# Kernel tuning notes

Measured on AMD Instinct MI355X. Metric: run time of the kernel, lower is better.

Reference implementation:

```python
import jax, jax.numpy as jnp
import numpy as np


def setup_inputs() -> dict:
    key = jax.random.key(0)
    ks = jax.random.split(key, 5)
    B, S, D, L = 16, 256, 768, 32
    return {
        "head": jax.random.normal(ks[0], (B, S, D), dtype=jnp.float32),
        "dep": jax.random.normal(ks[1], (B, S, D), dtype=jnp.float32),
        "label_U_diag": jax.random.normal(ks[2], (L, D), dtype=jnp.float32) * 0.02,
        "label_W": jax.random.normal(ks[3], (L, 2 * D), dtype=jnp.float32) * 0.02,
        "label_b": jax.random.normal(ks[4], (L,), dtype=jnp.float32) * 0.02,
    }


def reference(head, dep, label_U_diag, label_W, label_b):
    # head, dep: [b, s, d]; label_U_diag: [l, d]; label_W: [l, 2d]; label_b: [l]
    d = head.shape[-1]
    # Bilinear term with diagonal U: t1[b,l,i,o] = sum_d head[b,i,d]*U[l,d]*dep[b,o,d]
    t1 = jnp.einsum('bid,ld,bod->blio', head, label_U_diag, dep)
    # Linear term: W @ concat(head_i, dep_o) = W_h @ head_i + W_d @ dep_o
    W_h, W_d = label_W[:, :d], label_W[:, d:]
    t2_h = jnp.einsum('ld,bid->bli', W_h, head)  # [b, l, s]
    t2_d = jnp.einsum('ld,bod->blo', W_d, dep)   # [b, l, s]
    return t1 + t2_h[:, :, :, None] + t2_d[:, :, None, :] + label_b[None, :, None, None]
```

## Files before the change

kernel.cpp:

```cpp
#include <hip/hip_runtime.h>
#include <hip/hip_bf16.h>
#include <stdint.h>


#define B_ 16
#define S_ 256
#define D_ 768
#define L_ 32
#define KQ_ (D_ / 8)
#define NT_ 24

typedef unsigned short ushort_t;
typedef __attribute__((ext_vector_type(4))) float f32x4;
typedef __attribute__((ext_vector_type(8))) short s16x8;

__device__ __forceinline__ unsigned int pack_bf16(float f0, float f1) {
  unsigned int u0 = __builtin_bit_cast(unsigned int, f0) + 0x8000u;
  unsigned int u1 = __builtin_bit_cast(unsigned int, f1) + 0x8000u;
  return __builtin_amdgcn_perm(u1, u0, 0x07060302);
}

__global__ __launch_bounds__(256) void prep_kernel(
    const float* __restrict__ head, const float* __restrict__ dep,
    const float* __restrict__ labelW, ushort_t* __restrict__ depb,
    float* __restrict__ t2h, float* __restrict__ t2d) {
  const int wave = threadIdx.x >> 6;
  const int lane = threadIdx.x & 63;
  const int g = blockIdx.x * 4 + wave;
  const int sel = g >> 10;
  const int idx = g & 1023;
  const int b = idx >> 6;
  const int row0 = (idx & 63) * 4;
  const float* src = sel ? dep : head;
  float* t2x = sel ? t2d : t2h;
  const int d0 = lane * 12;

  float h[4][12];
  const float* rp = src + ((size_t)(b * S_ + row0)) * D_ + d0;
#pragma unroll
  for (int r = 0; r < 4; ++r) {
    float4 v0 = *(const float4*)(rp + (size_t)r * D_);
    float4 v1 = *(const float4*)(rp + (size_t)r * D_ + 4);
    float4 v2 = *(const float4*)(rp + (size_t)r * D_ + 8);
    h[r][0] = v0.x; h[r][1] = v0.y; h[r][2] = v0.z; h[r][3] = v0.w;
    h[r][4] = v1.x; h[r][5] = v1.y; h[r][6] = v1.z; h[r][7] = v1.w;
    h[r][8] = v2.x; h[r][9] = v2.y; h[r][10] = v2.z; h[r][11] = v2.w;
  }
  if (sel) {
    const size_t bb = (size_t)b * (KQ_ * S_ * 8);
    const int m = lane >> 1;
#pragma unroll
    for (int r = 0; r < 4; ++r) {
      const int col = row0 + r;
      unsigned int q0 = pack_bf16(h[r][0], h[r][1]);
      unsigned int q1 = pack_bf16(h[r][2], h[r][3]);
      unsigned int q2 = pack_bf16(h[r][4], h[r][5]);
      unsigned int q3 = pack_bf16(h[r][6], h[r][7]);
      unsigned int q4 = pack_bf16(h[r][8], h[r][9]);
      unsigned int q5 = pack_bf16(h[r][10], h[r][11]);
      if ((lane & 1) == 0) {
        uint4 a = {q0, q1, q2, q3};
        uint2 c = {q4, q5};
        *(uint4*)(depb + bb + ((size_t)(3 * m) * S_ + col) * 8) = a;
        *(uint2*)(depb + bb + ((size_t)(3 * m + 1) * S_ + col) * 8) = c;
      } else {
        uint2 c = {q0, q1};
        uint4 a = {q2, q3, q4, q5};
        *(uint2*)(depb + bb + ((size_t)(3 * m + 1) * S_ + col) * 8 + 4) = c;
        *(uint4*)(depb + bb + ((size_t)(3 * m + 2) * S_ + col) * 8) = a;
      }
    }
  }
  const float* wbase = labelW + sel * D_ + d0;
  for (int c = 0; c < 2; ++c) {
    float v[64];
#pragma unroll
    for (int j = 0; j < 64; ++j) v[j] = 0.f;
    const float* wc = wbase + (size_t)(c * 16) * (2 * D_);
#pragma unroll
    for (int lq = 0; lq < 16; ++lq) {
      const float* wp = wc + (size_t)lq * (2 * D_);
      float4 w0 = *(const float4*)(wp);
      float4 w1 = *(const float4*)(wp + 4);
      float4 w2 = *(const float4*)(wp + 8);
      float w[12] = {w0.x, w0.y, w0.z, w0.w, w1.x, w1.y, w1.z, w1.w,
                     w2.x, w2.y, w2.z, w2.w};
#pragma unroll
      for (int j = 0; j < 12; ++j) {
        v[lq * 4 + 0] += h[0][j] * w[j];
        v[lq * 4 + 1] += h[1][j] * w[j];
        v[lq * 4 + 2] += h[2][j] * w[j];
        v[lq * 4 + 3] += h[3][j] * w[j];
      }
    }
#pragma unroll
    for (int off = 32; off >= 1; off >>= 1) {
      const bool hi = (lane & off) != 0;
#pragma unroll
      for (int k = 0; k < 64; ++k) {
        if (k >= off) continue;
        float send = hi ? v[k] : v[k + off];
        float keep = hi ? v[k + off] : v[k];
        v[k] = keep + __shfl_xor(send, off);
      }
    }
    t2x[((size_t)(b * L_ + c * 16 + (lane >> 2))) * S_ + row0 + (lane & 3)] =
        v[0];
  }
}


#define SWZ(o) ((o) ^ ((((o) >> 10) & 3) << 4))

__global__ __launch_bounds__(256, 2) void main_kernel(
    const float* __restrict__ head, const ushort_t* __restrict__ depb,
    const float* __restrict__ U, const float* __restrict__ bias,
    const float* __restrict__ t2h, const float* __restrict__ t2d,
    float* __restrict__ out) {
  __shared__ __attribute__((aligned(16))) ushort_t As[2 * 128 * 32];
  __shared__ float T2[384];

  const int hw = blockIdx.x;
  const int bid = ((hw & 7) << 7) | (hw >> 3);
  const int ic = bid & 1;
  const int bl = bid >> 1;
  const int l = bl & (L_ - 1);
  const int b = bl >> 5;
  const int ti = ic * 128;
  const int t = threadIdx.x;
  const int lane = t & 63;
  const int wave = t >> 6;

  for (int i = t; i < 384; i += 256)
    T2[i] = (i < 128) ? t2h[((size_t)(b * L_ + l)) * S_ + ti + i]
                      : t2d[((size_t)(b * L_ + l)) * S_ + (i - 128)];
  const float bv = bias[l];

  const int row0 = t >> 2;
  const int kg = t & 3;
  const float* hp0 = head + ((size_t)(b * S_ + ti + row0)) * D_ + kg * 8;
  const float* hp1 = hp0 + (size_t)64 * D_;
  const float* Up = U + (size_t)l * D_ + kg * 8;
  const int awo0s = SWZ((kg * 128 + row0) * 8);
  const int awo1s = awo0s + 512;

  const int aros = SWZ(((lane >> 4) * 128 + (lane & 15)) * 8);

  const ushort_t* dfb = depb + (size_t)b * (KQ_ * S_ * 8) +
                        ((size_t)((lane >> 4) * 256 + wave * 64 + (lane & 15))) * 8;

  f32x4 acc[8][4];
#pragma unroll
  for (int i = 0; i < 8; ++i)
#pragma unroll
    for (int j = 0; j < 4; ++j) acc[i][j] = {0.f, 0.f, 0.f, 0.f};

  s16x8 bfA[4], bfB[4];

  {
    float4 h0 = *(const float4*)(hp0);
    float4 h1 = *(const float4*)(hp0 + 4);
    float4 h2 = *(const float4*)(hp1);
    float4 h3 = *(const float4*)(hp1 + 4);
    float4 u0 = *(const float4*)(Up);
    float4 u1 = *(const float4*)(Up + 4);
    uint4 w0, w1;
    w0.x = pack_bf16(h0.x * u0.x, h0.y * u0.y);
    w0.y = pack_bf16(h0.z * u0.z, h0.w * u0.w);
    w0.z = pack_bf16(h1.x * u1.x, h1.y * u1.y);
    w0.w = pack_bf16(h1.z * u1.z, h1.w * u1.w);
    w1.x = pack_bf16(h2.x * u0.x, h2.y * u0.y);
    w1.y = pack_bf16(h2.z * u0.z, h2.w * u0.w);
    w1.z = pack_bf16(h3.x * u1.x, h3.y * u1.y);
    w1.w = pack_bf16(h3.z * u1.z, h3.w * u1.w);
    *(uint4*)(As + awo0s) = w0;
    *(uint4*)(As + awo1s) = w1;
#pragma unroll
    for (int ct = 0; ct < 4; ++ct)
      bfA[ct] = *(const s16x8*)(dfb + ct * 128);
  }
  asm volatile("s_waitcnt lgkmcnt(0)" ::: "memory");
  __builtin_amdgcn_s_barrier();
  __builtin_amdgcn_sched_barrier(0);

#define ITER(PB, BFC, BFN, tcur)                                              \
  {                                                                           \
    int tn = (tcur) + 1;                                                      \
    if (tn == NT_) tn = 0;     \
    const float* hA = hp0 + tn * 32;                                          \
    const float* hB = hp1 + tn * 32;                                          \
    const float* uA = Up + tn * 32;                                           \
    float4 h0 = *(const float4*)(hA);                                         \
    float4 h1 = *(const float4*)(hA + 4);                                     \
    float4 h2 = *(const float4*)(hB);                                         \
    float4 h3 = *(const float4*)(hB + 4);                                     \
    float4 u0 = *(const float4*)(uA);                                         \
    float4 u1 = *(const float4*)(uA + 4);                                     \
    const ushort_t* dfn = dfb + (size_t)tn * 8192;                            \
    _Pragma("unroll") for (int ct = 0; ct < 4; ++ct)                          \
        BFN[ct] = *(const s16x8*)(dfn + ct * 128);                            \
    __builtin_amdgcn_sched_barrier(0);       \
    s16x8 af[8];                                                              \
    _Pragma("unroll") for (int rt = 0; rt < 8; ++rt)                          \
        af[rt] = *(const s16x8*)(As + (PB)*4096 + aros + rt * 128);           \
    __builtin_amdgcn_s_setprio(1);                                            \
    _Pragma("unroll") for (int rt = 0; rt < 8; ++rt)                          \
      _Pragma("unroll") for (int ct = 0; ct < 4; ++ct)                        \
          acc[rt][ct] = __builtin_amdgcn_mfma_f32_16x16x32_bf16(              \
              af[rt], BFC[ct], acc[rt][ct], 0, 0, 0);                         \
    __builtin_amdgcn_s_setprio(0);                                            \
    uint4 w0, w1;                                                             \
    w0.x = pack_bf16(h0.x * u0.x, h0.y * u0.y);                               \
    w0.y = pack_bf16(h0.z * u0.z, h0.w * u0.w);                               \
    w0.z = pack_bf16(h1.x * u1.x, h1.y * u1.y);                               \
    w0.w = pack_bf16(h1.z * u1.z, h1.w * u1.w);                               \
    w1.x = pack_bf16(h2.x * u0.x, h2.y * u0.y);                               \
    w1.y = pack_bf16(h2.z * u0.z, h2.w * u0.w);                               \
    w1.z = pack_bf16(h3.x * u1.x, h3.y * u1.y);                               \
    w1.w = pack_bf16(h3.z * u1.z, h3.w * u1.w);                               \
    ushort_t* aw = As + ((PB) ^ 1) * 4096;                                    \
    *(uint4*)(aw + awo0s) = w0;                                               \
    *(uint4*)(aw + awo1s) = w1;                                               \
    asm volatile("s_waitcnt lgkmcnt(0)" ::: "memory");                        \
    __builtin_amdgcn_s_barrier();                                             \
    __builtin_amdgcn_sched_barrier(0);                                        \
  }

  for (int tt = 0; tt < NT_; tt += 2) {
    ITER(0, bfA, bfB, tt);
    ITER(1, bfB, bfA, tt + 1);
  }
#undef ITER

  const int colg = lane & 15;
  const int rgrp = lane >> 4;
  float* ob = out + (((size_t)(b * L_ + l)) * S_ + ti) * S_;
#pragma unroll
  for (int rt = 0; rt < 8; ++rt) {
    const int r0 = rt * 16 + rgrp * 4;
#pragma unroll
    for (int ct = 0; ct < 4; ++ct) {
      const int c = wave * 64 + ct * 16 + colg;
      const float addc = T2[128 + c] + bv;
      float* p = ob + (size_t)r0 * S_ + c;
#pragma unroll
      for (int r = 0; r < 4; ++r)
        p[(size_t)r * S_] = acc[rt][ct][r] + T2[r0 + r] + addc;
    }
  }
}

extern "C" void kernel_launch(void* const* d_in, const int* in_sizes, int n_in,
                              void* d_out, int out_size, void* d_ws, size_t ws_size,
                              hipStream_t stream) {
  const float* head = (const float*)d_in[0];
  const float* dep = (const float*)d_in[1];
  const float* U = (const float*)d_in[2];
  const float* W = (const float*)d_in[3];
  const float* bias = (const float*)d_in[4];
  float* out = (float*)d_out;

  ushort_t* depb = (ushort_t*)d_ws;
  float* t2h = (float*)((char*)d_ws + (size_t)B_ * S_ * D_ * 2);
  float* t2d = t2h + (size_t)B_ * L_ * S_;

  prep_kernel<<<512, 256, 0, stream>>>(head, dep, W, depb, t2h, t2d);
  main_kernel<<<B_ * L_ * 2, 256, 0, stream>>>(head, depb, U, bias, t2h, t2d, out);
}
```

Baseline: 213.5 us.

## Double the K-step per iteration to halve barriers and drop LDS swizzle

```diff
diff --git a/kernel.cpp b/kernel.cpp
--- a/kernel.cpp
+++ b/kernel.cpp
@@ -8,7 +8,7 @@
 #define D_ 768
 #define L_ 32
 #define KQ_ (D_ / 8)
-#define NT_ 24
+#define NT_ 12
 
 typedef unsigned short ushort_t;
 typedef __attribute__((ext_vector_type(4))) float f32x4;
@@ -109,15 +109,12 @@
   }
 }
 
-
-#define SWZ(o) ((o) ^ ((((o) >> 10) & 3) << 4))
-
 __global__ __launch_bounds__(256, 2) void main_kernel(
     const float* __restrict__ head, const ushort_t* __restrict__ depb,
     const float* __restrict__ U, const float* __restrict__ bias,
     const float* __restrict__ t2h, const float* __restrict__ t2d,
     float* __restrict__ out) {
-  __shared__ __attribute__((aligned(16))) ushort_t As[2 * 128 * 32];
+  __shared__ __attribute__((aligned(16))) ushort_t As[2 * 8 * 128 * 8];
   __shared__ float T2[384];
 
   const int hw = blockIdx.x;
@@ -136,15 +133,13 @@
                       : t2d[((size_t)(b * L_ + l)) * S_ + (i - 128)];
   const float bv = bias[l];
 
-  const int row0 = t >> 2;
-  const int kg = t & 3;
-  const float* hp0 = head + ((size_t)(b * S_ + ti + row0)) * D_ + kg * 8;
-  const float* hp1 = hp0 + (size_t)64 * D_;
+  const int row0 = t >> 3;
+  const int kg = t & 7;
+  const float* hp = head + ((size_t)(b * S_ + ti + row0)) * D_ + kg * 8;
   const float* Up = U + (size_t)l * D_ + kg * 8;
-  const int awo0s = SWZ((kg * 128 + row0) * 8);
-  const int awo1s = awo0s + 512;
-
-  const int aros = SWZ(((lane >> 4) * 128 + (lane & 15)) * 8);
+  const int awo = (kg * 128 + row0) * 8;
+
+  const int aro = ((lane >> 4) * 128 + (lane & 15)) * 8;
 
   const ushort_t* dfb = depb + (size_t)b * (KQ_ * S_ * 8) +
                         ((size_t)((lane >> 4) * 256 + wave * 64 + (lane & 15))) * 8;
@@ -155,29 +150,54 @@
 #pragma unroll
     for (int j = 0; j < 4; ++j) acc[i][j] = {0.f, 0.f, 0.f, 0.f};
 
-  s16x8 bfA[4], bfB[4];
+  s16x8 bfA[8], bfB[8];
+
+#define PACK_WRITE_A(BUF)                                                     \
+  {                                                                           \
+    ushort_t* aw = As + (BUF) * 8192 + awo;                                   \
+    uint4 w;                                                                  \
+    w.x = pack_bf16(h00.x * u0.x, h00.y * u0.y);                              \
+    w.y = pack_bf16(h00.z * u0.z, h00.w * u0.w);                              \
+    w.z = pack_bf16(h01.x * u1.x, h01.y * u1.y);                              \
+    w.w = pack_bf16(h01.z * u1.z, h01.w * u1.w);                              \
+    *(uint4*)(aw) = w;                                                        \
+    w.x = pack_bf16(h10.x * u0.x, h10.y * u0.y);                              \
+    w.y = pack_bf16(h10.z * u0.z, h10.w * u0.w);                              \
+    w.z = pack_bf16(h11.x * u1.x, h11.y * u1.y);                              \
+    w.w = pack_bf16(h11.z * u1.z, h11.w * u1.w);                              \
+    *(uint4*)(aw + 256) = w;                                                  \
+    w.x = pack_bf16(h20.x * u0.x, h20.y * u0.y);                              \
+    w.y = pack_bf16(h20.z * u0.z, h20.w * u0.w);                              \
+    w.z = pack_bf16(h21.x * u1.x, h21.y * u1.y);                              \
+    w.w = pack_bf16(h21.z * u1.z, h21.w * u1.w);                              \
+    *(uint4*)(aw + 512) = w;                                                  \
+    w.x = pack_bf16(h30.x * u0.x, h30.y * u0.y);                              \
+    w.y = pack_bf16(h30.z * u0.z, h30.w * u0.w);                              \
+    w.z = pack_bf16(h31.x * u1.x, h31.y * u1.y);                              \
+    w.w = pack_bf16(h31.z * u1.z, h31.w * u1.w);                              \
+    *(uint4*)(aw + 768) = w;                                                  \
+  }
+
+#define LOAD_HU(tn)                                                           \
+    const float* hq = hp + (tn) * 64;                                         \
+    const float* uq = Up + (tn) * 64;                                         \
+    float4 h00 = *(const float4*)(hq);                                        \
+    float4 h01 = *(const float4*)(hq + 4);                                    \
+    float4 h10 = *(const float4*)(hq + (size_t)32 * D_);                      \
+    float4 h11 = *(const float4*)(hq + (size_t)32 * D_ + 4);                  \
+    float4 h20 = *(const float4*)(hq + (size_t)64 * D_);                      \
+    float4 h21 = *(const float4*)(hq + (size_t)64 * D_ + 4);                  \
+    float4 h30 = *(const float4*)(hq + (size_t)96 * D_);                      \
+    float4 h31 = *(const float4*)(hq + (size_t)96 * D_ + 4);                  \
+    float4 u0 = *(const float4*)(uq);                                         \
+    float4 u1 = *(const float4*)(uq + 4);
 
   {
-    float4 h0 = *(const float4*)(hp0);
-    float4 h1 = *(const float4*)(hp0 + 4);
-    float4 h2 = *(const float4*)(hp1);
-    float4 h3 = *(const float4*)(hp1 + 4);
-    float4 u0 = *(const float4*)(Up);
-    float4 u1 = *(const float4*)(Up + 4);
-    uint4 w0, w1;
-    w0.x = pack_bf16(h0.x * u0.x, h0.y * u0.y);
-    w0.y = pack_bf16(h0.z * u0.z, h0.w * u0.w);
-    w0.z = pack_bf16(h1.x * u1.x, h1.y * u1.y);
-    w0.w = pack_bf16(h1.z * u1.z, h1.w * u1.w);
-    w1.x = pack_bf16(h2.x * u0.x, h2.y * u0.y);
-    w1.y = pack_bf16(h2.z * u0.z, h2.w * u0.w);
-    w1.z = pack_bf16(h3.x * u1.x, h3.y * u1.y);
-    w1.w = pack_bf16(h3.z * u1.z, h3.w * u1.w);
-    *(uint4*)(As + awo0s) = w0;
-    *(uint4*)(As + awo1s) = w1;
-#pragma unroll
-    for (int ct = 0; ct < 4; ++ct)
-      bfA[ct] = *(const s16x8*)(dfb + ct * 128);
+    LOAD_HU(0)
+    PACK_WRITE_A(0)
+#pragma unroll
+    for (int j = 0; j < 8; ++j)
+      bfA[j] = *(const s16x8*)(dfb + (j >> 2) * 8192 + (j & 3) * 128);
   }
   asm volatile("s_waitcnt lgkmcnt(0)" ::: "memory");
   __builtin_amdgcn_s_barrier();
@@ -187,40 +207,30 @@
   {                                                                           \
     int tn = (tcur) + 1;                                                      \
     if (tn == NT_) tn = 0;     \
-    const float* hA = hp0 + tn * 32;                                          \
-    const float* hB = hp1 + tn * 32;                                          \
-    const float* uA = Up + tn * 32;                                           \
-    float4 h0 = *(const float4*)(hA);                                         \
-    float4 h1 = *(const float4*)(hA + 4);                                     \
-    float4 h2 = *(const float4*)(hB);                                         \
-    float4 h3 = *(const float4*)(hB + 4);                                     \
-    float4 u0 = *(const float4*)(uA);                                         \
-    float4 u1 = *(const float4*)(uA + 4);                                     \
-    const ushort_t* dfn = dfb + (size_t)tn * 8192;                            \
-    _Pragma("unroll") for (int ct = 0; ct < 4; ++ct)                          \
-        BFN[ct] = *(const s16x8*)(dfn + ct * 128);                            \
+    const ushort_t* dfn = dfb + (size_t)tn * 16384;                           \
+    _Pragma("unroll") for (int j = 0; j < 8; ++j)                             \
+        BFN[j] = *(const s16x8*)(dfn + (j >> 2) * 8192 + (j & 3) * 128);      \
+    LOAD_HU(tn)                                                               \
     __builtin_amdgcn_sched_barrier(0);       \
+    const ushort_t* arb = As + (PB) * 8192 + aro;                             \
     s16x8 af[8];                                                              \
     _Pragma("unroll") for (int rt = 0; rt < 8; ++rt)                          \
-        af[rt] = *(const s16x8*)(As + (PB)*4096 + aros + rt * 128);           \
+        af[rt] = *(const s16x8*)(arb + rt * 128);                             \
     __builtin_amdgcn_s_setprio(1);                                            \
     _Pragma("unroll") for (int rt = 0; rt < 8; ++rt)                          \
       _Pragma("unroll") for (int ct = 0; ct < 4; ++ct)                        \
           acc[rt][ct] = __builtin_amdgcn_mfma_f32_16x16x32_bf16(              \
               af[rt], BFC[ct], acc[rt][ct], 0, 0, 0);                         \
     __builtin_amdgcn_s_setprio(0);                                            \
-    uint4 w0, w1;                                                             \
-    w0.x = pack_bf16(h0.x * u0.x, h0.y * u0.y);                               \
-    w0.y = pack_bf16(h0.z * u0.z, h0.w * u0.w);                               \
-    w0.z = pack_bf16(h1.x * u1.x, h1.y * u1.y);                               \
-    w0.w = pack_bf16(h1.z * u1.z, h1.w * u1.w);                               \
-    w1.x = pack_bf16(h2.x * u0.x, h2.y * u0.y);                               \
-    w1.y = pack_bf16(h2.z * u0.z, h2.w * u0.w);                               \
-    w1.z = pack_bf16(h3.x * u1.x, h3.y * u1.y);                               \
-    w1.w = pack_bf16(h3.z * u1.z, h3.w * u1.w);                               \
-    ushort_t* aw = As + ((PB) ^ 1) * 4096;                                    \
-    *(uint4*)(aw + awo0s) = w0;                                               \
-    *(uint4*)(aw + awo1s) = w1;                                               \
+    _Pragma("unroll") for (int rt = 0; rt < 8; ++rt)                          \
+        af[rt] = *(const s16x8*)(arb + 4096 + rt * 128);                      \
+    __builtin_amdgcn_s_setprio(1);                                            \
+    _Pragma("unroll") for (int rt = 0; rt < 8; ++rt)                          \
+      _Pragma("unroll") for (int ct = 0; ct < 4; ++ct)                        \
+          acc[rt][ct] = __builtin_amdgcn_mfma_f32_16x16x32_bf16(              \
+              af[rt], BFC[4 + ct], acc[rt][ct], 0, 0, 0);                     \
+    __builtin_amdgcn_s_setprio(0);                                            \
+    PACK_WRITE_A((PB) ^ 1)                                                    \
     asm volatile("s_waitcnt lgkmcnt(0)" ::: "memory");                        \
     __builtin_amdgcn_s_barrier();                                             \
     __builtin_amdgcn_sched_barrier(0);                                        \
@@ -231,6 +241,8 @@
     ITER(1, bfB, bfA, tt + 1);
   }
 #undef ITER
+#undef LOAD_HU
+#undef PACK_WRITE_A
 
   const int colg = lane & 15;
   const int rgrp = lane >> 4;
```

Measured after the change: 250.7 us. 17.4% more time.

## Split output tile into 128x128 blocks with 2x2 wave layout for more occupancy

Applied to the files above, without the earlier changes.

```diff
diff --git a/kernel.cpp b/kernel.cpp
--- a/kernel.cpp
+++ b/kernel.cpp
@@ -112,28 +112,31 @@
 
 #define SWZ(o) ((o) ^ ((((o) >> 10) & 3) << 4))
 
-__global__ __launch_bounds__(256, 2) void main_kernel(
+__global__ __launch_bounds__(256, 3) void main_kernel(
     const float* __restrict__ head, const ushort_t* __restrict__ depb,
     const float* __restrict__ U, const float* __restrict__ bias,
     const float* __restrict__ t2h, const float* __restrict__ t2d,
     float* __restrict__ out) {
   __shared__ __attribute__((aligned(16))) ushort_t As[2 * 128 * 32];
-  __shared__ float T2[384];
+  __shared__ float T2[256];
 
   const int hw = blockIdx.x;
-  const int bid = ((hw & 7) << 7) | (hw >> 3);
-  const int ic = bid & 1;
-  const int bl = bid >> 1;
-  const int l = bl & (L_ - 1);
-  const int b = bl >> 5;
-  const int ti = ic * 128;
+  const int bid = ((hw & 7) << 8) | (hw >> 3);
+  const int oh = bid & 1;
+  const int ih = (bid >> 1) & 1;
+  const int l = (bid >> 2) & (L_ - 1);
+  const int b = bid >> 7;
+  const int ti = ih * 128;
+  const int to = oh * 128;
   const int t = threadIdx.x;
   const int lane = t & 63;
   const int wave = t >> 6;
-
-  for (int i = t; i < 384; i += 256)
+  const int m_base = (wave >> 1) * 64;
+  const int n_base = (wave & 1) * 64;
+
+  for (int i = t; i < 256; i += 256)
     T2[i] = (i < 128) ? t2h[((size_t)(b * L_ + l)) * S_ + ti + i]
-                      : t2d[((size_t)(b * L_ + l)) * S_ + (i - 128)];
+                      : t2d[((size_t)(b * L_ + l)) * S_ + to + (i - 128)];
   const float bv = bias[l];
 
   const int row0 = t >> 2;
@@ -144,14 +147,15 @@
   const int awo0s = SWZ((kg * 128 + row0) * 8);
   const int awo1s = awo0s + 512;
 
-  const int aros = SWZ(((lane >> 4) * 128 + (lane & 15)) * 8);
-
-  const ushort_t* dfb = depb + (size_t)b * (KQ_ * S_ * 8) +
-                        ((size_t)((lane >> 4) * 256 + wave * 64 + (lane & 15))) * 8;
-
-  f32x4 acc[8][4];
-#pragma unroll
-  for (int i = 0; i < 8; ++i)
+  const int aros = SWZ(((lane >> 4) * 128 + m_base + (lane & 15)) * 8);
+
+  const ushort_t* dfb =
+      depb + (size_t)b * (KQ_ * S_ * 8) +
+      ((size_t)((lane >> 4) * 256 + to + n_base + (lane & 15))) * 8;
+
+  f32x4 acc[4][4];
+#pragma unroll
+  for (int i = 0; i < 4; ++i)
 #pragma unroll
     for (int j = 0; j < 4; ++j) acc[i][j] = {0.f, 0.f, 0.f, 0.f};
 
@@ -200,15 +204,13 @@
     _Pragma("unroll") for (int ct = 0; ct < 4; ++ct)                          \
         BFN[ct] = *(const s16x8*)(dfn + ct * 128);                            \
     __builtin_amdgcn_sched_barrier(0);       \
-    s16x8 af[8];                                                              \
-    _Pragma("unroll") for (int rt = 0; rt < 8; ++rt)                          \
+    s16x8 af[4];                                                              \
+    _Pragma("unroll") for (int rt = 0; rt < 4; ++rt)                          \
         af[rt] = *(const s16x8*)(As + (PB)*4096 + aros + rt * 128);           \
-    __builtin_amdgcn_s_setprio(1);                                            \
-    _Pragma("unroll") for (int rt = 0; rt < 8; ++rt)                          \
+    _Pragma("unroll") for (int rt = 0; rt < 4; ++rt)                          \
       _Pragma("unroll") for (int ct = 0; ct < 4; ++ct)                        \
           acc[rt][ct] = __builtin_amdgcn_mfma_f32_16x16x32_bf16(              \
               af[rt], BFC[ct], acc[rt][ct], 0, 0, 0);                         \
-    __builtin_amdgcn_s_setprio(0);                                            \
     uint4 w0, w1;                                                             \
     w0.x = pack_bf16(h0.x * u0.x, h0.y * u0.y);                               \
     w0.y = pack_bf16(h0.z * u0.z, h0.w * u0.w);                               \
@@ -234,13 +236,13 @@
 
   const int colg = lane & 15;
   const int rgrp = lane >> 4;
-  float* ob = out + (((size_t)(b * L_ + l)) * S_ + ti) * S_;
-#pragma unroll
-  for (int rt = 0; rt < 8; ++rt) {
-    const int r0 = rt * 16 + rgrp * 4;
+  float* ob = out + (((size_t)(b * L_ + l)) * S_ + ti) * S_ + to;
+#pragma unroll
+  for (int rt = 0; rt < 4; ++rt) {
+    const int r0 = m_base + rt * 16 + rgrp * 4;
 #pragma unroll
     for (int ct = 0; ct < 4; ++ct) {
-      const int c = wave * 64 + ct * 16 + colg;
+      const int c = n_base + ct * 16 + colg;
       const float addc = T2[128 + c] + bv;
       float* p = ob + (size_t)r0 * S_ + c;
 #pragma unroll
@@ -265,5 +267,5 @@
   float* t2d = t2h + (size_t)B_ * L_ * S_;
 
   prep_kernel<<<512, 256, 0, stream>>>(head, dep, W, depb, t2h, t2d);
-  main_kernel<<<B_ * L_ * 2, 256, 0, stream>>>(head, depb, U, bias, t2h, t2d, out);
-}
+  main_kernel<<<B_ * L_ * 4, 256, 0, stream>>>(head, depb, U, bias, t2h, t2d, out);
+}
```

Result: slower. 232.9 us (+9.0%).

## Drop LDS staging of scaled head tile; build A fragments in registers with 8 waves

Applied to the files above, without the earlier changes.

```diff
diff --git a/kernel.cpp b/kernel.cpp
--- a/kernel.cpp
+++ b/kernel.cpp
@@ -110,14 +110,21 @@
 }
 
 
-#define SWZ(o) ((o) ^ ((((o) >> 10) & 3) << 4))
-
-__global__ __launch_bounds__(256, 2) void main_kernel(
+#define PACK1(DST, ha, hb, uu0, uu1)                                          \
+  {                                                                           \
+    uint4 w;                                                                  \
+    w.x = pack_bf16((ha).x * (uu0).x, (ha).y * (uu0).y);                      \
+    w.y = pack_bf16((ha).z * (uu0).z, (ha).w * (uu0).w);                      \
+    w.z = pack_bf16((hb).x * (uu1).x, (hb).y * (uu1).y);                      \
+    w.w = pack_bf16((hb).z * (uu1).z, (hb).w * (uu1).w);                      \
+    DST = __builtin_bit_cast(s16x8, w);                                       \
+  }
+
+__global__ __launch_bounds__(512, 2) void main_kernel(
     const float* __restrict__ head, const ushort_t* __restrict__ depb,
     const float* __restrict__ U, const float* __restrict__ bias,
     const float* __restrict__ t2h, const float* __restrict__ t2d,
     float* __restrict__ out) {
-  __shared__ __attribute__((aligned(16))) ushort_t As[2 * 128 * 32];
   __shared__ float T2[384];
 
   const int hw = blockIdx.x;
@@ -130,122 +137,101 @@
   const int t = threadIdx.x;
   const int lane = t & 63;
   const int wave = t >> 6;
-
-  for (int i = t; i < 384; i += 256)
+  const int rh = wave >> 2;
+  const int cg = wave & 3;
+
+  for (int i = t; i < 384; i += 512)
     T2[i] = (i < 128) ? t2h[((size_t)(b * L_ + l)) * S_ + ti + i]
                       : t2d[((size_t)(b * L_ + l)) * S_ + (i - 128)];
+  __syncthreads();
   const float bv = bias[l];
 
-  const int row0 = t >> 2;
-  const int kg = t & 3;
-  const float* hp0 = head + ((size_t)(b * S_ + ti + row0)) * D_ + kg * 8;
-  const float* hp1 = hp0 + (size_t)64 * D_;
+  const int colg = lane & 15;
+  const int kg = lane >> 4;
+
+  const float* hf =
+      head + ((size_t)(b * S_ + ti + rh * 64 + colg)) * D_ + kg * 8;
   const float* Up = U + (size_t)l * D_ + kg * 8;
-  const int awo0s = SWZ((kg * 128 + row0) * 8);
-  const int awo1s = awo0s + 512;
-
-  const int aros = SWZ(((lane >> 4) * 128 + (lane & 15)) * 8);
-
   const ushort_t* dfb = depb + (size_t)b * (KQ_ * S_ * 8) +
-                        ((size_t)((lane >> 4) * 256 + wave * 64 + (lane & 15))) * 8;
-
-  f32x4 acc[8][4];
-#pragma unroll
-  for (int i = 0; i < 8; ++i)
+                        ((size_t)(kg * 256 + cg * 64 + colg)) * 8;
+
+  f32x4 acc[4][4];
+#pragma unroll
+  for (int i = 0; i < 4; ++i)
 #pragma unroll
     for (int j = 0; j < 4; ++j) acc[i][j] = {0.f, 0.f, 0.f, 0.f};
 
-  s16x8 bfA[4], bfB[4];
+  s16x8 afA[4], afB[4], bfA[4], bfB[4];
 
   {
-    float4 h0 = *(const float4*)(hp0);
-    float4 h1 = *(const float4*)(hp0 + 4);
-    float4 h2 = *(const float4*)(hp1);
-    float4 h3 = *(const float4*)(hp1 + 4);
     float4 u0 = *(const float4*)(Up);
     float4 u1 = *(const float4*)(Up + 4);
-    uint4 w0, w1;
-    w0.x = pack_bf16(h0.x * u0.x, h0.y * u0.y);
-    w0.y = pack_bf16(h0.z * u0.z, h0.w * u0.w);
-    w0.z = pack_bf16(h1.x * u1.x, h1.y * u1.y);
-    w0.w = pack_bf16(h1.z * u1.z, h1.w * u1.w);
-    w1.x = pack_bf16(h2.x * u0.x, h2.y * u0.y);
-    w1.y = pack_bf16(h2.z * u0.z, h2.w * u0.w);
-    w1.z = pack_bf16(h3.x * u1.x, h3.y * u1.y);
-    w1.w = pack_bf16(h3.z * u1.z, h3.w * u1.w);
-    *(uint4*)(As + awo0s) = w0;
-    *(uint4*)(As + awo1s) = w1;
+    float4 h00 = *(const float4*)(hf);
+    float4 h01 = *(const float4*)(hf + 4);
+    float4 h10 = *(const float4*)(hf + 12288);
+    float4 h11 = *(const float4*)(hf + 12292);
+    float4 h20 = *(const float4*)(hf + 24576);
+    float4 h21 = *(const float4*)(hf + 24580);
+    float4 h30 = *(const float4*)(hf + 36864);
+    float4 h31 = *(const float4*)(hf + 36868);
 #pragma unroll
     for (int ct = 0; ct < 4; ++ct)
       bfA[ct] = *(const s16x8*)(dfb + ct * 128);
-  }
-  asm volatile("s_waitcnt lgkmcnt(0)" ::: "memory");
-  __builtin_amdgcn_s_barrier();
-  __builtin_amdgcn_sched_barrier(0);
-
-#define ITER(PB, BFC, BFN, tcur)                                              \
+    PACK1(afA[0], h00, h01, u0, u1)
+    PACK1(afA[1], h10, h11, u0, u1)
+    PACK1(afA[2], h20, h21, u0, u1)
+    PACK1(afA[3], h30, h31, u0, u1)
+  }
+
+#define ITER(AFC, AFN, BFC, BFN, tcur)                                        \
   {                                                                           \
     int tn = (tcur) + 1;                                                      \
     if (tn == NT_) tn = 0;     \
-    const float* hA = hp0 + tn * 32;                                          \
-    const float* hB = hp1 + tn * 32;                                          \
-    const float* uA = Up + tn * 32;                                           \
-    float4 h0 = *(const float4*)(hA);                                         \
-    float4 h1 = *(const float4*)(hA + 4);                                     \
-    float4 h2 = *(const float4*)(hB);                                         \
-    float4 h3 = *(const float4*)(hB + 4);                                     \
-    float4 u0 = *(const float4*)(uA);                                         \
-    float4 u1 = *(const float4*)(uA + 4);                                     \
+    const float* hq = hf + tn * 32;                                           \
+    float4 u0 = *(const float4*)(Up + tn * 32);                               \
+    float4 u1 = *(const float4*)(Up + tn * 32 + 4);                           \
+    float4 h00 = *(const float4*)(hq);                                        \
+    float4 h01 = *(const float4*)(hq + 4);                                    \
+    float4 h10 = *(const float4*)(hq + 12288);                                \
+    float4 h11 = *(const float4*)(hq + 12292);                                \
+    float4 h20 = *(const float4*)(hq + 24576);                                \
+    float4 h21 = *(const float4*)(hq + 24580);                                \
+    float4 h30 = *(const float4*)(hq + 36864);                                \
+    float4 h31 = *(const float4*)(hq + 36868);                                \
     const ushort_t* dfn = dfb + (size_t)tn * 8192;                            \
     _Pragma("unroll") for (int ct = 0; ct < 4; ++ct)                          \
         BFN[ct] = *(const s16x8*)(dfn + ct * 128);                            \
     __builtin_amdgcn_sched_barrier(0);       \
-    s16x8 af[8];                                                              \
-    _Pragma("unroll") for (int rt = 0; rt < 8; ++rt)                          \
-        af[rt] = *(const s16x8*)(As + (PB)*4096 + aros + rt * 128);           \
-    __builtin_amdgcn_s_setprio(1);                                            \
-    _Pragma("unroll") for (int rt = 0; rt < 8; ++rt)                          \
+    _Pragma("unroll") for (int rt = 0; rt < 4; ++rt)                          \
       _Pragma("unroll") for (int ct = 0; ct < 4; ++ct)                        \
           acc[rt][ct] = __builtin_amdgcn_mfma_f32_16x16x32_bf16(              \
-              af[rt], BFC[ct], acc[rt][ct], 0, 0, 0);                         \
-    __builtin_amdgcn_s_setprio(0);                                            \
-    uint4 w0, w1;                                                             \
-    w0.x = pack_bf16(h0.x * u0.x, h0.y * u0.y);                               \
-    w0.y = pack_bf16(h0.z * u0.z, h0.w * u0.w);                               \
-    w0.z = pack_bf16(h1.x * u1.x, h1.y * u1.y);                               \
-    w0.w = pack_bf16(h1.z * u1.z, h1.w * u1.w);                               \
-    w1.x = pack_bf16(h2.x * u0.x, h2.y * u0.y);                               \
-    w1.y = pack_bf16(h2.z * u0.z, h2.w * u0.w);                               \
-    w1.z = pack_bf16(h3.x * u1.x, h3.y * u1.y);                               \
-    w1.w = pack_bf16(h3.z * u1.z, h3.w * u1.w);                               \
-    ushort_t* aw = As + ((PB) ^ 1) * 4096;                                    \
-    *(uint4*)(aw + awo0s) = w0;                                               \
-    *(uint4*)(aw + awo1s) = w1;                                               \
-    asm volatile("s_waitcnt lgkmcnt(0)" ::: "memory");                        \
-    __builtin_amdgcn_s_barrier();                                             \
-    __builtin_amdgcn_sched_barrier(0);                                        \
+              AFC[rt], BFC[ct], acc[rt][ct], 0, 0, 0);                        \
+    PACK1(AFN[0], h00, h01, u0, u1)                                           \
+    PACK1(AFN[1], h10, h11, u0, u1)                                           \
+    PACK1(AFN[2], h20, h21, u0, u1)                                           \
+    PACK1(AFN[3], h30, h31, u0, u1)                                           \
   }
 
   for (int tt = 0; tt < NT_; tt += 2) {
-    ITER(0, bfA, bfB, tt);
-    ITER(1, bfB, bfA, tt + 1);
+    ITER(afA, afB, bfA, bfB, tt)
+    ITER(afB, afA, bfB, bfA, tt + 1)
   }
 #undef ITER
 
-  const int colg = lane & 15;
   const int rgrp = lane >> 4;
-  float* ob = out + (((size_t)(b * L_ + l)) * S_ + ti) * S_;
-#pragma unroll
-  for (int rt = 0; rt < 8; ++rt) {
+  float* ob =
+      out + (((size_t)(b * L_ + l)) * S_ + ti + rh * 64) * S_ + cg * 64;
+#pragma unroll
+  for (int rt = 0; rt < 4; ++rt) {
     const int r0 = rt * 16 + rgrp * 4;
 #pragma unroll
     for (int ct = 0; ct < 4; ++ct) {
-      const int c = wave * 64 + ct * 16 + colg;
-      const float addc = T2[128 + c] + bv;
+      const int c = ct * 16 + colg;
+      const float addc = T2[128 + cg * 64 + c] + bv;
       float* p = ob + (size_t)r0 * S_ + c;
 #pragma unroll
       for (int r = 0; r < 4; ++r)
-        p[(size_t)r * S_] = acc[rt][ct][r] + T2[r0 + r] + addc;
+        p[(size_t)r * S_] = acc[rt][ct][r] + T2[rh * 64 + r0 + r] + addc;
     }
   }
 }
@@ -265,5 +251,5 @@
   float* t2d = t2h + (size_t)B_ * L_ * S_;
 
   prep_kernel<<<512, 256, 0, stream>>>(head, dep, W, depb, t2h, t2d);
-  main_kernel<<<B_ * L_ * 2, 256, 0, stream>>>(head, depb, U, bias, t2h, t2d, out);
-}
+  main_kernel<<<B_ * L_ * 2, 512, 0, stream>>>(head, depb, U, bias, t2h, t2d, out);
+}
```

Result: slower. 371.8 us (+74.1%).
